# Kernel optimization log

Hardware: AMD Instinct MI355X
Metric: run time of the kernel (lower is better)

The kernel has to match this reference:

```python
import jax, jax.numpy as jnp
import numpy as np

B, N, ND, HD = 8, 512, 128, 256
NUM_OPS, NUM_PARAMS = 64, 16


def setup_inputs() -> dict:
    key = jax.random.key(0)
    ks = iter(jax.random.split(key, 80))
    def nrm(shape, s=0.02):
        return jax.random.normal(next(ks), shape, dtype=jnp.float32) * s
    inp = {}
    inp['node_features'] = jax.random.normal(next(ks), (B, N, ND), dtype=jnp.float32)
    inp['adjacency'] = (jax.random.uniform(next(ks), (B, N, N)) < 0.1).astype(jnp.float32)
    inp['mask'] = jnp.ones((B, N), jnp.float32)
    inp['op_types'] = jnp.zeros((B, N, NUM_OPS), jnp.int32)  # only its shape is used (T = N)
    # GNN layer params: linear (out,in)+bias, attention linear (1, 2*out)+bias
    for i, ind in zip((1, 2, 3), (ND, HD, HD)):
        inp[f'g{i}_w'] = nrm((HD, ind)); inp[f'g{i}_b'] = nrm((HD,))
        inp[f'g{i}_aw'] = nrm((1, 2 * HD)); inp[f'g{i}_ab'] = nrm((1,))
    # 2-layer bidirectional LSTM; single fused bias (= b_ih + b_hh), gate order i,f,g,o
    for l, ind in ((0, HD), (1, 2 * HD)):
        for d in 'fb':
            inp[f'wih{l}{d}'] = nrm((4 * HD, ind))
            inp[f'whh{l}{d}'] = nrm((4 * HD, HD))
            inp[f'b{l}{d}'] = nrm((4 * HD,))
    # MLP heads (dropout is identity in eval)
    for name, outd in (('op', NUM_OPS), ('pp', NUM_PARAMS), ('sk', 128), ('nd', ND)):
        ind = HD if name == 'nd' else 2 * HD
        inp[f'{name}_w1'] = nrm((HD, ind)); inp[f'{name}_b1'] = nrm((HD,))
        inp[f'{name}_w2'] = nrm((outd, HD)); inp[f'{name}_b2'] = nrm((outd,))
    return inp


def gnn(x, adj, mask, w, b, aw, ab):
    # Faithful to: sigmoid(Linear(cat[h_i, h_j])) — factored as per-node projections
    h = x @ w.T + b                      # (B,N,D)
    D = h.shape[-1]
    si = h @ aw[0, :D] + ab[0]           # (B,N) row contribution (+bias once)
    sj = h @ aw[0, D:]                   # (B,N) col contribution
    score = jax.nn.sigmoid(si[:, :, None] + sj[:, None, :])  # (B,N,N)
    score = score * adj * mask[:, :, None] * mask[:, None, :]
    w_att = score / (score.sum(-1, keepdims=True) + 1e-8)
    return jnp.einsum('bij,bjd->bid', w_att, h) * mask[:, :, None]


def lstm_dir(x, wih, whh, b, reverse):
    # x: (B,T,In); returns (B,T,H), outputs aligned with input positions
    xs = jnp.swapaxes(x, 0, 1)
    Bc, H = x.shape[0], whh.shape[1]
    pre = xs @ wih.T + b                 # (T,B,4H) input projection hoisted out of scan
    def step(carry, p):
        h, c = carry
        g = p + h @ whh.T
        i, f, gg, o = jnp.split(g, 4, -1)
        c = jax.nn.sigmoid(f) * c + jax.nn.sigmoid(i) * jnp.tanh(gg)
        h = jax.nn.sigmoid(o) * jnp.tanh(c)
        return (h, c), h
    init = (jnp.zeros((Bc, H), x.dtype), jnp.zeros((Bc, H), x.dtype))
    _, ys = jax.lax.scan(step, init, pre, reverse=reverse)
    return jnp.swapaxes(ys, 0, 1)


def bidir(x, wf, hf, bf, wb, hb, bb):
    return jnp.concatenate([lstm_dir(x, wf, hf, bf, False),
                            lstm_dir(x, wb, hb, bb, True)], -1)


def mlp(x, w1, b1, w2, b2):
    return jax.nn.relu(x @ w1.T + b1) @ w2.T + b2


def reference(node_features, adjacency, mask, op_types,
              g1_w, g1_b, g1_aw, g1_ab, g2_w, g2_b, g2_aw, g2_ab,
              g3_w, g3_b, g3_aw, g3_ab,
              wih0f, whh0f, b0f, wih0b, whh0b, b0b,
              wih1f, whh1f, b1f, wih1b, whh1b, b1b,
              op_w1, op_b1, op_w2, op_b2, pp_w1, pp_b1, pp_w2, pp_b2,
              sk_w1, sk_b1, sk_w2, sk_b2, nd_w1, nd_b1, nd_w2, nd_b2):
    h = jax.nn.relu(gnn(node_features, adjacency, mask, g1_w, g1_b, g1_aw, g1_ab))
    h = jax.nn.relu(gnn(h, adjacency, mask, g2_w, g2_b, g2_aw, g2_ab))
    h = gnn(h, adjacency, mask, g3_w, g3_b, g3_aw, g3_ab)
    # mask is all-ones -> pack_padded_sequence == plain full-length LSTM, T == N
    x = bidir(h, wih0f, whh0f, b0f, wih0b, whh0b, b0b)
    x = bidir(x, wih1f, whh1f, b1f, wih1b, whh1b, b1b)
    op_pred = mlp(x, op_w1, op_b1, op_w2, op_b2)
    param_pred = mlp(x, pp_w1, pp_b1, pp_w2, pp_b2)
    sketch_pred = mlp(x, sk_w1, sk_b1, sk_w2, sk_b2)
    node_pred = mlp(h, nd_w1, nd_b1, nd_w2, nd_b2)
    return op_pred, param_pred, sketch_pred, node_pred
```

## Files before the change

### kernel.cpp

```cpp
#include <hip/hip_runtime.h>

#define BB   8
#define NN   512
#define NDIM 128
#define HDIM 256
#define TT   512

__device__ __forceinline__ float sigmoidf_(float x) { return 1.0f / (1.0f + __expf(-x)); }
__device__ __forceinline__ float tanhf_(float x) { float e = __expf(2.0f * x); return 1.0f - 2.0f / (e + 1.0f); }

typedef _Float16 half2v __attribute__((ext_vector_type(2)));
typedef unsigned int uint4v __attribute__((ext_vector_type(4)));
typedef short bf16x8 __attribute__((ext_vector_type(8)));
typedef float f32x4 __attribute__((ext_vector_type(4)));
__device__ __forceinline__ float fdot2_(unsigned int w, unsigned int h, float acc) {
    return __builtin_amdgcn_fdot2(__builtin_bit_cast(half2v, w),
                                  __builtin_bit_cast(half2v, h), acc, false);
}
__device__ __forceinline__ unsigned short f2bf_(float x) {
    unsigned int u = __builtin_bit_cast(unsigned int, x);
    return (unsigned short)((u + 0x7FFFu + ((u >> 16) & 1u)) >> 16);
}

template<int RELU>
__global__ __launch_bounds__(256) void gemm_nt(const float* __restrict__ X,
    const float* __restrict__ W, const float* __restrict__ bias,
    float* __restrict__ Y, int M, int K, int Nn)
{
    __shared__ float Xs[16][68];
    __shared__ float Ws[16][68];
    const int tid = threadIdx.x;
    const int m0 = blockIdx.y << 6;
    const int n0 = blockIdx.x << 6;
    const int lr = tid >> 2;
    const int lc = (tid & 3) << 2;
    const int tm = (tid >> 4) << 2;
    const int tn = (tid & 15) << 2;

    float acc[4][4] = {{0.f,0.f,0.f,0.f},{0.f,0.f,0.f,0.f},{0.f,0.f,0.f,0.f},{0.f,0.f,0.f,0.f}};

    const float* Xp = X + (size_t)(m0 + lr) * K + lc;
    const bool wok = (n0 + lr) < Nn;
    const float* Wp = wok ? (W + (size_t)(n0 + lr) * K + lc) : W;

    for (int k0 = 0; k0 < K; k0 += 16) {
        float4 xv = *(const float4*)(Xp + k0);
        float4 wv = *(const float4*)(Wp + k0);
        if (!wok) wv = make_float4(0.f, 0.f, 0.f, 0.f);
        __syncthreads();
        Xs[lc+0][lr]=xv.x; Xs[lc+1][lr]=xv.y; Xs[lc+2][lr]=xv.z; Xs[lc+3][lr]=xv.w;
        Ws[lc+0][lr]=wv.x; Ws[lc+1][lr]=wv.y; Ws[lc+2][lr]=wv.z; Ws[lc+3][lr]=wv.w;
        __syncthreads();
        #pragma unroll
        for (int kk = 0; kk < 16; ++kk) {
            const float4 a = *(const float4*)(&Xs[kk][tm]);
            const float4 b = *(const float4*)(&Ws[kk][tn]);
            acc[0][0] += a.x*b.x; acc[0][1] += a.x*b.y; acc[0][2] += a.x*b.z; acc[0][3] += a.x*b.w;
            acc[1][0] += a.y*b.x; acc[1][1] += a.y*b.y; acc[1][2] += a.y*b.z; acc[1][3] += a.y*b.w;
            acc[2][0] += a.z*b.x; acc[2][1] += a.z*b.y; acc[2][2] += a.z*b.z; acc[2][3] += a.z*b.w;
            acc[3][0] += a.w*b.x; acc[3][1] += a.w*b.y; acc[3][2] += a.w*b.z; acc[3][3] += a.w*b.w;
        }
    }
    const int nc = n0 + tn;
    if (nc >= Nn) return;
    float4 bv = make_float4(0.f, 0.f, 0.f, 0.f);
    if (bias) bv = *(const float4*)(bias + nc);
    #pragma unroll
    for (int i = 0; i < 4; ++i) {
        float4 o;
        o.x = acc[i][0] + bv.x; o.y = acc[i][1] + bv.y;
        o.z = acc[i][2] + bv.z; o.w = acc[i][3] + bv.w;
        if (RELU) { o.x=fmaxf(o.x,0.f); o.y=fmaxf(o.y,0.f); o.z=fmaxf(o.z,0.f); o.w=fmaxf(o.w,0.f); }
        *(float4*)(Y + (size_t)(m0 + tm + i) * Nn + nc) = o;
    }
}

template<int RELU>
__global__ __launch_bounds__(256) void gemm_nt_mfma(
    const unsigned short* __restrict__ X, const unsigned short* __restrict__ W,
    const float* __restrict__ bias, float* __restrict__ Y, int K, int Nn)
{
    __shared__ unsigned short As[128][56];
    __shared__ unsigned short Bs[128][56];
    const int tid = threadIdx.x;
    const int m0 = blockIdx.y << 7;
    const int n0 = blockIdx.x << 7;
    const int wid = tid >> 6, lane = tid & 63;
    const int wm = (wid >> 1) << 6;
    const int wn = (wid & 1) << 6;
    const int sr = tid >> 2;
    const int sc = (tid & 3) << 3;

    f32x4 acc[4][4] = {};

    const int fr = lane & 15;
    const int kg = (lane >> 4) << 3;

    for (int k0 = 0; k0 < K; k0 += 32) {
        uint4 a0 = *(const uint4*)(X + (size_t)(m0 + sr) * K + k0 + sc);
        uint4 a1 = *(const uint4*)(X + (size_t)(m0 + sr + 64) * K + k0 + sc);
        uint4 b0 = *(const uint4*)(W + (size_t)(n0 + sr) * K + k0 + sc);
        uint4 b1 = *(const uint4*)(W + (size_t)(n0 + sr + 64) * K + k0 + sc);
        __syncthreads();
        *(uint4*)&As[sr][sc] = a0; *(uint4*)&As[sr + 64][sc] = a1;
        *(uint4*)&Bs[sr][sc] = b0; *(uint4*)&Bs[sr + 64][sc] = b1;
        __syncthreads();
        bf16x8 af[4], bf[4];
        #pragma unroll
        for (int i = 0; i < 4; ++i) {
            af[i] = *(const bf16x8*)&As[wm + i * 16 + fr][kg];
            bf[i] = *(const bf16x8*)&Bs[wn + i * 16 + fr][kg];
        }
        #pragma unroll
        for (int i = 0; i < 4; ++i)
            #pragma unroll
            for (int j = 0; j < 4; ++j)
                acc[i][j] = __builtin_amdgcn_mfma_f32_16x16x32_bf16(af[i], bf[j], acc[i][j], 0, 0, 0);
    }

    const int cr = (lane >> 4) << 2;
    const int cc = lane & 15;
    #pragma unroll
    for (int i = 0; i < 4; ++i) {
        #pragma unroll
        for (int j = 0; j < 4; ++j) {
            const int col = n0 + wn + j * 16 + cc;
            const float bv = bias ? bias[col] : 0.f;
            #pragma unroll
            for (int r = 0; r < 4; ++r) {
                const int row = m0 + wm + i * 16 + cr + r;
                float v = acc[i][j][r] + bv;
                if (RELU) v = fmaxf(v, 0.f);
                Y[(size_t)row * Nn + col] = v;
            }
        }
    }
}

template<int RELU>
__global__ __launch_bounds__(256) void gemm_nn_mask(const float* __restrict__ A,
    const float* __restrict__ Hm, const float* __restrict__ mask,
    float* __restrict__ Y, int M, int K, int Nn)
{
    const int b = blockIdx.z;
    A  += (size_t)b * M * K;
    Hm += (size_t)b * K * Nn;
    Y  += (size_t)b * M * Nn;
    __shared__ float As[16][68];
    __shared__ float Hs[16][68];
    const int tid = threadIdx.x;
    const int m0 = blockIdx.y << 6;
    const int n0 = blockIdx.x << 6;
    const int lr = tid >> 2;
    const int lc = (tid & 3) << 2;
    const int hr = tid >> 4;
    const int hc = (tid & 15) << 2;
    const int tm = (tid >> 4) << 2;
    const int tn = (tid & 15) << 2;

    float acc[4][4] = {{0.f,0.f,0.f,0.f},{0.f,0.f,0.f,0.f},{0.f,0.f,0.f,0.f},{0.f,0.f,0.f,0.f}};

    for (int k0 = 0; k0 < K; k0 += 16) {
        float4 av = *(const float4*)(A + (size_t)(m0 + lr) * K + k0 + lc);
        float4 hv = *(const float4*)(Hm + (size_t)(k0 + hr) * Nn + n0 + hc);
        __syncthreads();
        As[lc+0][lr]=av.x; As[lc+1][lr]=av.y; As[lc+2][lr]=av.z; As[lc+3][lr]=av.w;
        *(float4*)(&Hs[hr][hc]) = hv;
        __syncthreads();
        #pragma unroll
        for (int kk = 0; kk < 16; ++kk) {
            const float4 a = *(const float4*)(&As[kk][tm]);
            const float4 h = *(const float4*)(&Hs[kk][tn]);
            acc[0][0] += a.x*h.x; acc[0][1] += a.x*h.y; acc[0][2] += a.x*h.z; acc[0][3] += a.x*h.w;
            acc[1][0] += a.y*h.x; acc[1][1] += a.y*h.y; acc[1][2] += a.y*h.z; acc[1][3] += a.y*h.w;
            acc[2][0] += a.z*h.x; acc[2][1] += a.z*h.y; acc[2][2] += a.z*h.z; acc[2][3] += a.z*h.w;
            acc[3][0] += a.w*h.x; acc[3][1] += a.w*h.y; acc[3][2] += a.w*h.z; acc[3][3] += a.w*h.w;
        }
    }
    #pragma unroll
    for (int i = 0; i < 4; ++i) {
        const float mk = mask[b * M + m0 + tm + i];
        float4 o;
        o.x = acc[i][0]*mk; o.y = acc[i][1]*mk; o.z = acc[i][2]*mk; o.w = acc[i][3]*mk;
        if (RELU) { o.x=fmaxf(o.x,0.f); o.y=fmaxf(o.y,0.f); o.z=fmaxf(o.z,0.f); o.w=fmaxf(o.w,0.f); }
        *(float4*)(Y + (size_t)(m0 + tm + i) * Nn + n0 + tn) = o;
    }
}

__global__ __launch_bounds__(256) void attn_sisj(const float* __restrict__ h,
    const float* __restrict__ aw, const float* __restrict__ ab,
    float* __restrict__ si, float* __restrict__ sj)
{
    const int lane = threadIdx.x & 63;
    const int row  = (blockIdx.x << 2) + (threadIdx.x >> 6);
    const float4 hv = ((const float4*)(h + (size_t)row * HDIM))[lane];
    const float4 a1 = ((const float4*)aw)[lane];
    const float4 a2 = ((const float4*)(aw + HDIM))[lane];
    float s1 = hv.x*a1.x + hv.y*a1.y + hv.z*a1.z + hv.w*a1.w;
    float s2 = hv.x*a2.x + hv.y*a2.y + hv.z*a2.z + hv.w*a2.w;
    #pragma unroll
    for (int off = 32; off > 0; off >>= 1) {
        s1 += __shfl_down(s1, off);
        s2 += __shfl_down(s2, off);
    }
    if (lane == 0) { si[row] = s1 + ab[0]; sj[row] = s2; }
}

__global__ __launch_bounds__(512) void attn_score(const float* __restrict__ si,
    const float* __restrict__ sj, const float* __restrict__ adj,
    const float* __restrict__ mask, float* __restrict__ watt)
{
    const int bi = blockIdx.x;
    const int b  = bi >> 9;
    const int j  = threadIdx.x;
    const float s0 = si[bi];
    const float mi = mask[bi];
    float s = sigmoidf_(s0 + sj[(b << 9) + j]) * adj[(size_t)bi * NN + j] * mi * mask[(b << 9) + j];
    float t = s;
    #pragma unroll
    for (int off = 32; off > 0; off >>= 1) t += __shfl_down(t, off);
    __shared__ float red[8];
    const int lane = j & 63, wv = j >> 6;
    if (lane == 0) red[wv] = t;
    __syncthreads();
    if (j == 0) {
        float tot = 0.f;
        #pragma unroll
        for (int w = 0; w < 8; ++w) tot += red[w];
        red[0] = 1.0f / (tot + 1e-8f);
    }
    __syncthreads();
    watt[(size_t)bi * NN + j] = s * red[0];
}

__global__ __launch_bounds__(256) void pack_f16(const float* __restrict__ src,
    unsigned int* __restrict__ dst, int n)
{
    int i = blockIdx.x * 256 + threadIdx.x;
    if (i < n) {
        float2 v = ((const float2*)src)[i];
        _Float16 a = (_Float16)v.x, b = (_Float16)v.y;
        unsigned short ua = *(unsigned short*)&a, ub = *(unsigned short*)&b;
        dst[i] = (unsigned int)ua | ((unsigned int)ub << 16);
    }
}

__global__ __launch_bounds__(256) void pack3_bf16(
    const float* __restrict__ s0, unsigned short* __restrict__ d0, int n0,
    const float* __restrict__ s1, unsigned short* __restrict__ d1, int n1,
    const float* __restrict__ s2, unsigned short* __restrict__ d2, int n2)
{
    int i = (blockIdx.x * 256 + threadIdx.x) * 4;
    const float* s; unsigned short* d; int l;
    if (i < n0) { s = s0; d = d0; l = i; }
    else if (i < n0 + n1) { s = s1; d = d1; l = i - n0; }
    else if (i < n0 + n1 + n2) { s = s2; d = d2; l = i - n0 - n1; }
    else return;
    float4 v = *(const float4*)(s + l);
    ushort4 o;
    o.x = f2bf_(v.x); o.y = f2bf_(v.y); o.z = f2bf_(v.z); o.w = f2bf_(v.w);
    *(ushort4*)(d + l) = o;
}

__global__ __launch_bounds__(1024) __attribute__((amdgpu_waves_per_eu(4, 4)))
void lstm_scan7(
    const float* __restrict__ pre_f, const float* __restrict__ pre_b,
    const unsigned int* __restrict__ w16_f, const unsigned int* __restrict__ w16_b,
    float* __restrict__ out)
{
    __shared__ uint4v lw4[8 * 1024];
    __shared__ float g_s[1024];
    __shared__ unsigned int h2[128];

    const int chain = blockIdx.x;
    const int batch = chain >> 1;
    const int dir   = chain & 1;
    const float* pre = dir ? pre_b : pre_f;
    const unsigned int* w = dir ? w16_b : w16_f;
    const int t0 = threadIdx.x;

    const uint4v* wr = (const uint4v*)(w + (size_t)t0 * 128);

    #pragma unroll
    for (int i = 0; i < 8; ++i) lw4[i * 1024 + t0] = wr[24 + i];

#define WD(i) uint4v W##i = wr[i];
    WD(0) WD(1) WD(2) WD(3) WD(4) WD(5) WD(6) WD(7) WD(8) WD(9) WD(10) WD(11)
    WD(12) WD(13) WD(14) WD(15) WD(16) WD(17) WD(18) WD(19) WD(20) WD(21) WD(22) WD(23)
#undef WD
#define PIN_ALL \
    { \
        asm volatile("" : "+v"(W0)); asm volatile("" : "+v"(W1)); \
        asm volatile("" : "+v"(W2)); asm volatile("" : "+v"(W3)); \
        asm volatile("" : "+v"(W4)); asm volatile("" : "+v"(W5)); \
        asm volatile("" : "+v"(W6)); asm volatile("" : "+v"(W7)); \
        asm volatile("" : "+v"(W8)); asm volatile("" : "+v"(W9)); \
        asm volatile("" : "+v"(W10)); asm volatile("" : "+v"(W11)); \
        asm volatile("" : "+v"(W12)); asm volatile("" : "+v"(W13)); \
        asm volatile("" : "+v"(W14)); asm volatile("" : "+v"(W15)); \
        asm volatile("" : "+v"(W16)); asm volatile("" : "+v"(W17)); \
        asm volatile("" : "+v"(W18)); asm volatile("" : "+v"(W19)); \
        asm volatile("" : "+v"(W20)); asm volatile("" : "+v"(W21)); \
        asm volatile("" : "+v"(W22)); asm volatile("" : "+v"(W23)); \
    }
    PIN_ALL

    if (t0 < 128) h2[t0] = 0u;
    float c = 0.f;

    const int tt0 = dir ? (TT - 1) : 0;
    const long pstep = dir ? -1024 : 1024;
    const long ostep = dir ? -512 : 512;
    const float* pp = pre + ((size_t)batch * TT + tt0) * 1024 + t0;
    float* op = out + ((size_t)batch * TT + tt0) * 512 + dir * 256 + t0;
    float pv = *pp; pp += pstep;
    __syncthreads();

    for (int t = 0; t < TT; ++t) {
        PIN_ALL

        float pv_n = 0.f;
        if (t + 1 < TT) pv_n = *pp;
        pp += pstep;

        float a0 = 0.f, a1 = 0.f, a2 = 0.f, a3 = 0.f;
        const uint4v* h4 = (const uint4v*)h2;
#define DOT(i) { const uint4v hv = h4[i]; \
        a0 = fdot2_(W##i.x, hv.x, a0); a1 = fdot2_(W##i.y, hv.y, a1); \
        a2 = fdot2_(W##i.z, hv.z, a2); a3 = fdot2_(W##i.w, hv.w, a3); }
        DOT(0) DOT(1) DOT(2) DOT(3) DOT(4) DOT(5) DOT(6) DOT(7)
        DOT(8) DOT(9) DOT(10) DOT(11) DOT(12) DOT(13) DOT(14) DOT(15)
        DOT(16) DOT(17) DOT(18) DOT(19) DOT(20) DOT(21) DOT(22) DOT(23)
#undef DOT
        #pragma unroll
        for (int i = 0; i < 8; ++i) {
            const uint4v wv = lw4[i * 1024 + t0];
            const uint4v hv = h4[24 + i];
            a0 = fdot2_(wv.x, hv.x, a0); a1 = fdot2_(wv.y, hv.y, a1);
            a2 = fdot2_(wv.z, hv.z, a2); a3 = fdot2_(wv.w, hv.w, a3);
        }
        g_s[t0] = (a0 + a1) + (a2 + a3) + pv;
        __syncthreads();
        if (t0 < 256) {
            const float ig = sigmoidf_(g_s[t0]);
            const float fg = sigmoidf_(g_s[256 + t0]);
            const float gg = tanhf_(g_s[512 + t0]);
            const float og = sigmoidf_(g_s[768 + t0]);
            c = fg * c + ig * gg;
            const float h = og * tanhf_(c);
            *op = h;
            op += ostep;
            _Float16 hh = (_Float16)h;
            ((unsigned short*)h2)[t0] = *(unsigned short*)&hh;
        }
        pv = pv_n;
        __syncthreads();
    }
#undef PIN_ALL
}


extern "C" void kernel_launch(void* const* d_in, const int* in_sizes, int n_in,
                              void* d_out, int out_size, void* d_ws, size_t ws_size,
                              hipStream_t stream)
{
    const float* nf   = (const float*)d_in[0];
    const float* adj  = (const float*)d_in[1];
    const float* mask = (const float*)d_in[2];
    const float* g_w[3]  = {(const float*)d_in[4],  (const float*)d_in[8],  (const float*)d_in[12]};
    const float* g_b[3]  = {(const float*)d_in[5],  (const float*)d_in[9],  (const float*)d_in[13]};
    const float* g_aw[3] = {(const float*)d_in[6],  (const float*)d_in[10], (const float*)d_in[14]};
    const float* g_ab[3] = {(const float*)d_in[7],  (const float*)d_in[11], (const float*)d_in[15]};
    const float* wih0f = (const float*)d_in[16]; const float* whh0f = (const float*)d_in[17]; const float* b0f = (const float*)d_in[18];
    const float* wih0b = (const float*)d_in[19]; const float* whh0b = (const float*)d_in[20]; const float* b0b = (const float*)d_in[21];
    const float* wih1f = (const float*)d_in[22]; const float* whh1f = (const float*)d_in[23]; const float* b1f = (const float*)d_in[24];
    const float* wih1b = (const float*)d_in[25]; const float* whh1b = (const float*)d_in[26]; const float* b1b = (const float*)d_in[27];

    float* ws = (float*)d_ws;
    float* bufA = ws;
    float* bufB = bufA + 1048576;
    float* bufC = bufB + 1048576;
    float* si   = bufC + 1048576;
    float* sj   = si + 4096;
    float* out0 = sj + 4096;
    float* out1 = out0 + 2097152;
    float* P0   = out1 + 2097152;
    float* P1   = P0 + 4194304;
    float* watt = P0;
    unsigned int* w16_0f = (unsigned int*)bufB;
    unsigned int* w16_0b = w16_0f + 131072;
    unsigned int* w16_1f = w16_0b + 131072;
    unsigned int* w16_1b = w16_1f + 131072;
    unsigned short* nfp   = (unsigned short*)P1;
    unsigned short* bufBp = (unsigned short*)(P1 + 262144);
    unsigned short* gwp1  = (unsigned short*)(P1 + 786432);
    unsigned short* gwp2  = (unsigned short*)(P1 + 802816);
    unsigned short* gwp3  = (unsigned short*)(P1 + 835584);
    unsigned short* bufCp  = (unsigned short*)bufA;
    unsigned short* out0p  = (unsigned short*)bufA;
    unsigned short* wih0fp = (unsigned short*)out1;
    unsigned short* wih0bp = (unsigned short*)(out1 + 131072);
    unsigned short* wih1fp = (unsigned short*)(out1 + 262144);
    unsigned short* wih1bp = (unsigned short*)(out1 + 524288);
    unsigned short* out1p  = (unsigned short*)P0;
    unsigned short* bufCp2 = (unsigned short*)(P0 + 1048576);
    unsigned short* opw1p  = (unsigned short*)(P0 + 1572864);
    unsigned short* ppw1p  = (unsigned short*)(P0 + 1638400);
    unsigned short* skw1p  = (unsigned short*)(P0 + 1703936);
    unsigned short* ndw1p  = (unsigned short*)(P0 + 1769472);

    const int MR = BB * NN;
    dim3 blk(256);

    pack3_bf16<<<dim3(608), blk, 0, stream>>>(nf, nfp, 524288,
                                              g_w[0], gwp1, 32768,
                                              g_w[1], gwp2, 65536);
    auto run_attn = [&](int li, float* ob, bool relu) {
        attn_sisj<<<dim3(MR / 4), blk, 0, stream>>>(bufA, g_aw[li], g_ab[li], si, sj);
        attn_score<<<dim3(MR), dim3(512), 0, stream>>>(si, sj, adj, mask, watt);
        if (relu)
            gemm_nn_mask<1><<<dim3(HDIM / 64, NN / 64, BB), blk, 0, stream>>>(watt, bufA, mask, ob, NN, NN, HDIM);
        else
            gemm_nn_mask<0><<<dim3(HDIM / 64, NN / 64, BB), blk, 0, stream>>>(watt, bufA, mask, ob, NN, NN, HDIM);
    };
    gemm_nt_mfma<0><<<dim3(2, 32), blk, 0, stream>>>(nfp, gwp1, g_b[0], bufA, NDIM, HDIM);
    run_attn(0, bufB, true);
    pack3_bf16<<<dim3(1088), blk, 0, stream>>>(bufB, bufBp, 1048576,
                                               g_w[2], gwp3, 65536,
                                               (const float*)0, (unsigned short*)0, 0);
    gemm_nt_mfma<0><<<dim3(2, 32), blk, 0, stream>>>(bufBp, gwp2, g_b[1], bufA, HDIM, HDIM);
    run_attn(1, bufB, true);
    pack3_bf16<<<dim3(1024), blk, 0, stream>>>(bufB, bufBp, 1048576,
                                               (const float*)0, (unsigned short*)0, 0,
                                               (const float*)0, (unsigned short*)0, 0);
    gemm_nt_mfma<0><<<dim3(2, 32), blk, 0, stream>>>(bufBp, gwp3, g_b[2], bufA, HDIM, HDIM);
    run_attn(2, bufC, false);

    pack_f16<<<dim3(512), blk, 0, stream>>>(whh0f, w16_0f, 131072);
    pack_f16<<<dim3(512), blk, 0, stream>>>(whh0b, w16_0b, 131072);
    pack_f16<<<dim3(512), blk, 0, stream>>>(whh1f, w16_1f, 131072);
    pack_f16<<<dim3(512), blk, 0, stream>>>(whh1b, w16_1b, 131072);

    pack3_bf16<<<dim3(1536), blk, 0, stream>>>(bufC, bufCp, 1048576,
                                               wih0f, wih0fp, 262144,
                                               wih0b, wih0bp, 262144);
    gemm_nt_mfma<0><<<dim3(8, 32), blk, 0, stream>>>(bufCp, wih0fp, b0f, P0, HDIM, 1024);
    gemm_nt_mfma<0><<<dim3(8, 32), blk, 0, stream>>>(bufCp, wih0bp, b0b, P1, HDIM, 1024);
    lstm_scan7<<<dim3(16), dim3(1024), 0, stream>>>(P0, P1, w16_0f, w16_0b, out0);

    pack3_bf16<<<dim3(3072), blk, 0, stream>>>(out0, out0p, 2097152,
                                               wih1f, wih1fp, 524288,
                                               wih1b, wih1bp, 524288);
    gemm_nt_mfma<0><<<dim3(8, 32), blk, 0, stream>>>(out0p, wih1fp, b1f, P0, 512, 1024);
    gemm_nt_mfma<0><<<dim3(8, 32), blk, 0, stream>>>(out0p, wih1bp, b1b, P1, 512, 1024);
    lstm_scan7<<<dim3(16), dim3(1024), 0, stream>>>(P0, P1, w16_1f, w16_1b, out1);

    float* out = (float*)d_out;
    pack3_bf16<<<dim3(3200), blk, 0, stream>>>(out1, out1p, 2097152,
                                               bufC, bufCp2, 1048576,
                                               (const float*)d_in[28], opw1p, 131072);
    pack3_bf16<<<dim3(320), blk, 0, stream>>>((const float*)d_in[32], ppw1p, 131072,
                                              (const float*)d_in[36], skw1p, 131072,
                                              (const float*)d_in[40], ndw1p, 65536);
    gemm_nt_mfma<1><<<dim3(2, 32), blk, 0, stream>>>(out1p, opw1p, (const float*)d_in[29], bufA, 512, 256);
    gemm_nt<0><<<dim3(1, MR / 64), blk, 0, stream>>>(bufA, (const float*)d_in[30], (const float*)d_in[31], out, MR, 256, 64);
    gemm_nt_mfma<1><<<dim3(2, 32), blk, 0, stream>>>(out1p, ppw1p, (const float*)d_in[33], bufA, 512, 256);
    gemm_nt<0><<<dim3(1, MR / 64), blk, 0, stream>>>(bufA, (const float*)d_in[34], (const float*)d_in[35], out + 262144, MR, 256, 16);
    gemm_nt_mfma<1><<<dim3(2, 32), blk, 0, stream>>>(out1p, skw1p, (const float*)d_in[37], bufA, 512, 256);
    gemm_nt<0><<<dim3(2, MR / 64), blk, 0, stream>>>(bufA, (const float*)d_in[38], (const float*)d_in[39], out + 327680, MR, 256, 128);
    gemm_nt_mfma<1><<<dim3(2, 32), blk, 0, stream>>>(bufCp2, ndw1p, (const float*)d_in[41], bufA, 256, 256);
    gemm_nt<0><<<dim3(2, MR / 64), blk, 0, stream>>>(bufA, (const float*)d_in[42], (const float*)d_in[43], out + 851968, MR, 256, 128);
}
```

Baseline: 2.365 ms.

## Split each LSTM recurrence chain across two workgroups with flag-based hidden-state exchange

Each LSTM direction/batch chain now runs on two 512-thread workgroups instead of one 1024-thread workgroup. Each workgroup owns half the hidden units across all four gates. The halves swap fp16 hidden states through a double-buffered global buffer, using release/acquire flags and a spin-wait every timestep. This spreads the serial recurrence over more CUs, with less per-CU work and more weights held in registers and LDS per thread. The cost is cross-CU synchronisation latency on every one of the 512 steps, plus a zeroing kernel before each scan. The spin-wait also requires both workgroups of a chain to be co-resident, or it will deadlock.

```diff
diff --git a/kernel.cpp b/kernel.cpp
--- a/kernel.cpp
+++ b/kernel.cpp
@@ -20,6 +20,10 @@
 __device__ __forceinline__ unsigned short f2bf_(float x) {
     unsigned int u = __builtin_bit_cast(unsigned int, x);
     return (unsigned short)((u + 0x7FFFu + ((u >> 16) & 1u)) >> 16);
+}
+__device__ __forceinline__ unsigned short f2h_(float x) {
+    _Float16 h = (_Float16)x;
+    return *(unsigned short*)&h;
 }
 
 template<int RELU>
@@ -239,9 +243,7 @@
     int i = blockIdx.x * 256 + threadIdx.x;
     if (i < n) {
         float2 v = ((const float2*)src)[i];
-        _Float16 a = (_Float16)v.x, b = (_Float16)v.y;
-        unsigned short ua = *(unsigned short*)&a, ub = *(unsigned short*)&b;
-        dst[i] = (unsigned int)ua | ((unsigned int)ub << 16);
+        dst[i] = (unsigned int)f2h_(v.x) | ((unsigned int)f2h_(v.y) << 16);
     }
 }
 
@@ -262,57 +264,66 @@
     *(ushort4*)(d + l) = o;
 }
 
-__global__ __launch_bounds__(1024) __attribute__((amdgpu_waves_per_eu(4, 4)))
-void lstm_scan7(
+__global__ __launch_bounds__(256) void zero_ws(unsigned int* __restrict__ p, int n)
+{
+    for (int i = threadIdx.x + blockIdx.x * 256; i < n; i += 256 * gridDim.x) p[i] = 0u;
+}
+
+__global__ __launch_bounds__(512) __attribute__((amdgpu_waves_per_eu(2, 2)))
+void lstm_scan8(
     const float* __restrict__ pre_f, const float* __restrict__ pre_b,
     const unsigned int* __restrict__ w16_f, const unsigned int* __restrict__ w16_b,
-    float* __restrict__ out)
-{
-    __shared__ uint4v lw4[8 * 1024];
-    __shared__ float g_s[1024];
+    float* __restrict__ out, unsigned int* __restrict__ hb, int* __restrict__ fl)
+{
+    __shared__ uint4v lw4[16 * 512];
+    __shared__ float g_s[512];
     __shared__ unsigned int h2[128];
 
-    const int chain = blockIdx.x;
+    const int chain = blockIdx.x & 15;
+    const int sl    = blockIdx.x >> 4;
     const int batch = chain >> 1;
     const int dir   = chain & 1;
     const float* pre = dir ? pre_b : pre_f;
     const unsigned int* w = dir ? w16_b : w16_f;
-    const int t0 = threadIdx.x;
-
-    const uint4v* wr = (const uint4v*)(w + (size_t)t0 * 128);
+    const int t0   = threadIdx.x;
+    const int gate = t0 >> 7;
+    const int uoff = t0 & 127;
+    const int grow = gate * 256 + sl * 128 + uoff;
+
+    const uint4v* wr = (const uint4v*)(w + (size_t)grow * 128);
 
     #pragma unroll
-    for (int i = 0; i < 8; ++i) lw4[i * 1024 + t0] = wr[24 + i];
+    for (int i = 0; i < 16; ++i) lw4[i * 512 + t0] = wr[i];
 
 #define WD(i) uint4v W##i = wr[i];
-    WD(0) WD(1) WD(2) WD(3) WD(4) WD(5) WD(6) WD(7) WD(8) WD(9) WD(10) WD(11)
-    WD(12) WD(13) WD(14) WD(15) WD(16) WD(17) WD(18) WD(19) WD(20) WD(21) WD(22) WD(23)
+    WD(16) WD(17) WD(18) WD(19) WD(20) WD(21) WD(22) WD(23)
+    WD(24) WD(25) WD(26) WD(27) WD(28) WD(29) WD(30) WD(31)
 #undef WD
 #define PIN_ALL \
     { \
-        asm volatile("" : "+v"(W0)); asm volatile("" : "+v"(W1)); \
-        asm volatile("" : "+v"(W2)); asm volatile("" : "+v"(W3)); \
-        asm volatile("" : "+v"(W4)); asm volatile("" : "+v"(W5)); \
-        asm volatile("" : "+v"(W6)); asm volatile("" : "+v"(W7)); \
-        asm volatile("" : "+v"(W8)); asm volatile("" : "+v"(W9)); \
-        asm volatile("" : "+v"(W10)); asm volatile("" : "+v"(W11)); \
-        asm volatile("" : "+v"(W12)); asm volatile("" : "+v"(W13)); \
-        asm volatile("" : "+v"(W14)); asm volatile("" : "+v"(W15)); \
         asm volatile("" : "+v"(W16)); asm volatile("" : "+v"(W17)); \
         asm volatile("" : "+v"(W18)); asm volatile("" : "+v"(W19)); \
         asm volatile("" : "+v"(W20)); asm volatile("" : "+v"(W21)); \
         asm volatile("" : "+v"(W22)); asm volatile("" : "+v"(W23)); \
+        asm volatile("" : "+v"(W24)); asm volatile("" : "+v"(W25)); \
+        asm volatile("" : "+v"(W26)); asm volatile("" : "+v"(W27)); \
+        asm volatile("" : "+v"(W28)); asm volatile("" : "+v"(W29)); \
+        asm volatile("" : "+v"(W30)); asm volatile("" : "+v"(W31)); \
     }
     PIN_ALL
 
     if (t0 < 128) h2[t0] = 0u;
-    float c = 0.f;
+    float c0 = 0.f, c1 = 0.f;
+
+    int* myflag = fl + chain * 2 + sl;
+    int* pflag  = fl + chain * 2 + (sl ^ 1);
+    unsigned int* hb_c = hb + chain * 128;
 
     const int tt0 = dir ? (TT - 1) : 0;
     const long pstep = dir ? -1024 : 1024;
     const long ostep = dir ? -512 : 512;
-    const float* pp = pre + ((size_t)batch * TT + tt0) * 1024 + t0;
-    float* op = out + ((size_t)batch * TT + tt0) * 512 + dir * 256 + t0;
+    const float* pp = pre + ((size_t)batch * TT + tt0) * 1024 + grow;
+    float* op = out + ((size_t)batch * TT + tt0) * 512 + dir * 256 + sl * 128 + 2 * t0;
     float pv = *pp; pp += pstep;
     __syncthreads();
 
@@ -325,36 +336,58 @@
 
         float a0 = 0.f, a1 = 0.f, a2 = 0.f, a3 = 0.f;
         const uint4v* h4 = (const uint4v*)h2;
+        #pragma unroll
+        for (int i = 0; i < 16; ++i) {
+            const uint4v wv = lw4[i * 512 + t0];
+            const uint4v hv = h4[i];
+            a0 = fdot2_(wv.x, hv.x, a0); a1 = fdot2_(wv.y, hv.y, a1);
+            a2 = fdot2_(wv.z, hv.z, a2); a3 = fdot2_(wv.w, hv.w, a3);
+        }
 #define DOT(i) { const uint4v hv = h4[i]; \
         a0 = fdot2_(W##i.x, hv.x, a0); a1 = fdot2_(W##i.y, hv.y, a1); \
         a2 = fdot2_(W##i.z, hv.z, a2); a3 = fdot2_(W##i.w, hv.w, a3); }
-        DOT(0) DOT(1) DOT(2) DOT(3) DOT(4) DOT(5) DOT(6) DOT(7)
-        DOT(8) DOT(9) DOT(10) DOT(11) DOT(12) DOT(13) DOT(14) DOT(15)
         DOT(16) DOT(17) DOT(18) DOT(19) DOT(20) DOT(21) DOT(22) DOT(23)
+        DOT(24) DOT(25) DOT(26) DOT(27) DOT(28) DOT(29) DOT(30) DOT(31)
 #undef DOT
-        #pragma unroll
-        for (int i = 0; i < 8; ++i) {
-            const uint4v wv = lw4[i * 1024 + t0];
-            const uint4v hv = h4[24 + i];
-            a0 = fdot2_(wv.x, hv.x, a0); a1 = fdot2_(wv.y, hv.y, a1);
-            a2 = fdot2_(wv.z, hv.z, a2); a3 = fdot2_(wv.w, hv.w, a3);
-        }
         g_s[t0] = (a0 + a1) + (a2 + a3) + pv;
         __syncthreads();
-        if (t0 < 256) {
-            const float ig = sigmoidf_(g_s[t0]);
-            const float fg = sigmoidf_(g_s[256 + t0]);
-            const float gg = tanhf_(g_s[512 + t0]);
-            const float og = sigmoidf_(g_s[768 + t0]);
-            c = fg * c + ig * gg;
-            const float h = og * tanhf_(c);
-            *op = h;
+
+        if (t0 < 64) {
+            const int u2 = 2 * t0;
+            const float ia = sigmoidf_(g_s[u2]),       ib = sigmoidf_(g_s[u2 + 1]);
+            const float fa = sigmoidf_(g_s[128 + u2]), fb = sigmoidf_(g_s[128 + u2 + 1]);
+            const float ga = tanhf_(g_s[256 + u2]),    gb = tanhf_(g_s[256 + u2 + 1]);
+            const float oa = sigmoidf_(g_s[384 + u2]), ob = sigmoidf_(g_s[384 + u2 + 1]);
+            c0 = fa * c0 + ia * ga;
+            c1 = fb * c1 + ib * gb;
+            const float h0 = oa * tanhf_(c0);
+            const float h1 = ob * tanhf_(c1);
+            *(float2*)op = make_float2(h0, h1);
             op += ostep;
-            _Float16 hh = (_Float16)h;
-            ((unsigned short*)h2)[t0] = *(unsigned short*)&hh;
+            const unsigned int packed = (unsigned int)f2h_(h0) | ((unsigned int)f2h_(h1) << 16);
+            h2[sl * 64 + t0] = packed;
+            if (t + 1 < TT)
+                __hip_atomic_store(&hb_c[(size_t)((t + 1) & 1) * 2048 + sl * 64 + t0],
+                                   packed, __ATOMIC_RELAXED, __HIP_MEMORY_SCOPE_AGENT);
+        }
+        __syncthreads();
+
+        if (t + 1 < TT) {
+            if (t0 == 0)
+                __hip_atomic_store(myflag, t + 1, __ATOMIC_RELEASE, __HIP_MEMORY_SCOPE_AGENT);
+            if (t0 == 64) {
+                while (__hip_atomic_load(pflag, __ATOMIC_ACQUIRE,
+                                         __HIP_MEMORY_SCOPE_AGENT) < t + 1) { }
+            }
+            __syncthreads();
+            if (t0 < 64) {
+                h2[(sl ^ 1) * 64 + t0] =
+                    __hip_atomic_load(&hb_c[(size_t)((t + 1) & 1) * 2048 + (sl ^ 1) * 64 + t0],
+                                      __ATOMIC_RELAXED, __HIP_MEMORY_SCOPE_AGENT);
+            }
+            __syncthreads();
         }
         pv = pv_n;
-        __syncthreads();
     }
 #undef PIN_ALL
 }
@@ -391,6 +424,9 @@
     unsigned int* w16_0b = w16_0f + 131072;
     unsigned int* w16_1f = w16_0b + 131072;
     unsigned int* w16_1b = w16_1f + 131072;
+    unsigned int* hb = (unsigned int*)bufB + 524288;
+    int*          fl = (int*)(hb + 4096);
+    const int SYNC_U32 = 4096 + 32;
     unsigned short* nfp   = (unsigned short*)P1;
     unsigned short* bufBp = (unsigned short*)(P1 + 262144);
     unsigned short* gwp1  = (unsigned short*)(P1 + 786432);
@@ -446,14 +482,16 @@
                                                wih0b, wih0bp, 262144);
     gemm_nt_mfma<0><<<dim3(8, 32), blk, 0, stream>>>(bufCp, wih0fp, b0f, P0, HDIM, 1024);
     gemm_nt_mfma<0><<<dim3(8, 32), blk, 0, stream>>>(bufCp, wih0bp, b0b, P1, HDIM, 1024);
-    lstm_scan7<<<dim3(16), dim3(1024), 0, stream>>>(P0, P1, w16_0f, w16_0b, out0);
+    zero_ws<<<dim3(8), blk, 0, stream>>>(hb, SYNC_U32);
+    lstm_scan8<<<dim3(32), dim3(512), 0, stream>>>(P0, P1, w16_0f, w16_0b, out0, hb, fl);
 
     pack3_bf16<<<dim3(3072), blk, 0, stream>>>(out0, out0p, 2097152,
                                                wih1f, wih1fp, 524288,
                                                wih1b, wih1bp, 524288);
     gemm_nt_mfma<0><<<dim3(8, 32), blk, 0, stream>>>(out0p, wih1fp, b1f, P0, 512, 1024);
     gemm_nt_mfma<0><<<dim3(8, 32), blk, 0, stream>>>(out0p, wih1bp, b1b, P1, 512, 1024);
-    lstm_scan7<<<dim3(16), dim3(1024), 0, stream>>>(P0, P1, w16_1f, w16_1b, out1);
+    zero_ws<<<dim3(8), blk, 0, stream>>>(hb, SYNC_U32);
+    lstm_scan8<<<dim3(32), dim3(512), 0, stream>>>(P0, P1, w16_1f, w16_1b, out1, hb, fl);
 
     float* out = (float*)d_out;
     pack3_bf16<<<dim3(3200), blk, 0, stream>>>(out1, out1p, 2097152,
```

New measurement: 4.093 ms. 1.73x slower.
